# Optimization experiments

Measured on AMD Instinct MI355X. Metric: run time of the kernel, lower is better.

## Reference

```python
import jax, jax.numpy as jnp
import numpy as np

B, CIN, COUT, H, W, K, KH, KW = 32, 256, 256, 56, 56, 4, 3, 3
STRIDE, PAD = (1, 1), [(1, 1), (1, 1)]


def setup_inputs() -> dict:
    key = jax.random.key(0)
    ks = jax.random.split(key, 8)
    s_w = 1.0 / np.sqrt(CIN * KH * KW)
    return {
        "x": jax.random.normal(ks[0], (B, CIN, H, W), jnp.float32),
        "weight": jax.random.normal(ks[1], (K, COUT, CIN, KH, KW), jnp.float32) * s_w,
        "bias": jax.random.normal(ks[2], (K, COUT), jnp.float32) * s_w,
        "fc1_w": jax.random.normal(ks[3], (K, CIN), jnp.float32) / np.sqrt(CIN),
        "fc1_b": jax.random.normal(ks[4], (K,), jnp.float32) * 0.01,
        "fc2_w": jax.random.normal(ks[5], (K, K), jnp.float32) / np.sqrt(K),
        "fc2_b": jax.random.normal(ks[6], (K,), jnp.float32) * 0.01,
    }


def reference(x, weight, bias, fc1_w, fc1_b, fc2_w, fc2_b):
    # Attention2D: global avg pool -> 1x1 conv (dense) -> relu -> 1x1 conv -> softmax
    pooled = x.mean(axis=(2, 3))                                  # [B, CIN]
    a = jax.nn.relu(jnp.einsum('bc,kc->bk', pooled, fc1_w) + fc1_b)
    att = jax.nn.softmax(jnp.einsum('bk,jk->bj', a, fc2_w) + fc2_b, axis=1)  # [B, K]

    # Aggregate per-sample weights/bias over K experts
    agg_w = jnp.einsum('bk,koihw->boihw', att, weight)            # [B, COUT, CIN, KH, KW]
    agg_b = att @ bias                                            # [B, COUT]

    # Per-sample conv == grouped conv with groups=B in the torch original
    def conv_one(xi, wi):
        return jax.lax.conv_general_dilated(
            xi[None], wi, window_strides=STRIDE, padding=PAD,
            dimension_numbers=('NCHW', 'OIHW', 'NCHW'))[0]

    out = jax.vmap(conv_one)(x, agg_w)                            # [B, COUT, H, W]
    return out + agg_b[:, :, None, None]
```

## Files before the change

### kernel.cpp

```cpp
#include <hip/hip_runtime.h>
#include <hip/hip_bf16.h>
#include <stdint.h>

#define BB   32
#define CIN  256
#define COUT 256
#define HH   56
#define WW   56
#define HW   3136
#define KEXP 4
#define HP   58

typedef __attribute__((ext_vector_type(8))) short  short8;
typedef __attribute__((ext_vector_type(4))) float  floatx4;

__device__ __forceinline__ unsigned short f2bf(float f) {
    uint32_t u = __float_as_uint(f);
    u = (u + 0x7fffu + ((u >> 16) & 1u)) >> 16;
    return (unsigned short)u;
}
__device__ __forceinline__ float bf2f(unsigned short s) {
    return __uint_as_float(((uint32_t)s) << 16);
}
__device__ __forceinline__ uint32_t pack2(float a, float b) {
    return (uint32_t)f2bf(a) | ((uint32_t)f2bf(b) << 16);
}

__device__ __forceinline__ void async_copy16(const void* gsrc, void* ldst) {
    __builtin_amdgcn_global_load_lds(
        (const __attribute__((address_space(1))) unsigned int*)gsrc,
        (__attribute__((address_space(3))) unsigned int*)ldst, 16, 0, 0);
}

__global__ __launch_bounds__(256) void transpose_pool_kernel(
    const float* __restrict__ x,
    unsigned short* __restrict__ xt,
    float* __restrict__ partial)
{
    __shared__ unsigned short tile[CIN * 62];
    const int bx  = blockIdx.x;
    const int b   = bx / HH;
    const int h   = bx % HH;
    const int tid = threadIdx.x;

    const float* xb = x + (size_t)b * CIN * HW + h * WW;

    for (int i = tid; i < CIN * 14; i += 256) {
        const int c  = i / 14;
        const int wv = i % 14;
        const float4 v = *(const float4*)(xb + (size_t)c * HW + wv * 4);
        uint32_t* p = (uint32_t*)&tile[c * 62 + wv * 4];
        p[0] = pack2(v.x, v.y);
        p[1] = pack2(v.z, v.w);
    }
    __syncthreads();

    {
        float s = 0.f;
        #pragma unroll 8
        for (int i = 0; i < WW; ++i) s += bf2f(tile[tid * 62 + i]);
        partial[((size_t)b * HH + h) * CIN + tid] = s;
    }

    unsigned short* row = xt + (((size_t)b * HP + (h + 1)) * HP) * CIN;
    for (int j = tid; j < WW * 128; j += 256) {
        const int w  = j >> 7;
        const int c2 = (j & 127) * 2;
        const uint32_t v = (uint32_t)tile[c2 * 62 + w]
                         | ((uint32_t)tile[(c2 + 1) * 62 + w] << 16);
        *(uint32_t*)&row[(w + 1) * CIN + c2] = v;
    }

    if (tid < 128) {
        ((uint32_t*)&row[0])[tid]          = 0u;
        ((uint32_t*)&row[57 * CIN])[tid]   = 0u;
    }
    if (h == 0) {
        uint32_t* r0  = (uint32_t*)(xt + ((size_t)b * HP + 0)  * HP * CIN);
        uint32_t* r57 = (uint32_t*)(xt + ((size_t)b * HP + 57) * HP * CIN);
        for (int i = tid; i < HP * 128; i += 256) { r0[i] = 0u; r57[i] = 0u; }
    }
}

__global__ __launch_bounds__(256) void attn_kernel(
    const float* __restrict__ partial,
    const float* __restrict__ fc1w,
    const float* __restrict__ fc1b,
    const float* __restrict__ fc2w,
    const float* __restrict__ fc2b,
    float* __restrict__ att)
{
    __shared__ float pl[CIN];
    const int b   = blockIdx.x;
    const int tid = threadIdx.x;

    float s = 0.f;
    const float* pp = partial + (size_t)b * HH * CIN + tid;
    #pragma unroll 8
    for (int h = 0; h < HH; ++h) s += pp[h * CIN];
    pl[tid] = s * (1.0f / (float)HW);
    __syncthreads();

    if (tid < 64) {
        const int lane = tid;
        float sk[KEXP] = {0.f, 0.f, 0.f, 0.f};
        #pragma unroll
        for (int c0 = 0; c0 < CIN; c0 += 64) {
            const float p = pl[c0 + lane];
            #pragma unroll
            for (int k = 0; k < KEXP; ++k) sk[k] += p * fc1w[k * CIN + c0 + lane];
        }
        #pragma unroll
        for (int off = 32; off > 0; off >>= 1) {
            #pragma unroll
            for (int k = 0; k < KEXP; ++k) sk[k] += __shfl_down(sk[k], off);
        }
        if (lane == 0) {
            float a[KEXP];
            #pragma unroll
            for (int k = 0; k < KEXP; ++k) a[k] = fmaxf(sk[k] + fc1b[k], 0.f);
            float z[KEXP], m = -1e30f;
            #pragma unroll
            for (int j = 0; j < KEXP; ++j) {
                float t = fc2b[j];
                #pragma unroll
                for (int k = 0; k < KEXP; ++k) t += a[k] * fc2w[j * KEXP + k];
                z[j] = t;
                m = fmaxf(m, t);
            }
            float den = 0.f;
            #pragma unroll
            for (int j = 0; j < KEXP; ++j) { z[j] = expf(z[j] - m); den += z[j]; }
            const float inv = 1.0f / den;
            #pragma unroll
            for (int j = 0; j < KEXP; ++j) att[b * KEXP + j] = z[j] * inv;
        }
    }
}

__global__ __launch_bounds__(256) void aggw_kernel(
    const float* __restrict__ weight,
    const float* __restrict__ bias,
    const float* __restrict__ att,
    unsigned short* __restrict__ aggw,
    float* __restrict__ aggb)
{
    __shared__ float accw[CIN * 9];
    const int bx  = blockIdx.x;
    const int o   = bx >> 2;
    const int b0  = (bx & 3) * 8;
    const int tid = threadIdx.x;

    float wreg[KEXP][9];
    #pragma unroll
    for (int k = 0; k < KEXP; ++k) {
        const float* wk = weight + (size_t)(k * COUT + o) * (CIN * 9);
        #pragma unroll
        for (int j = 0; j < 9; ++j) wreg[k][j] = wk[j * 256 + tid];
    }
    float bvals[KEXP];
    #pragma unroll
    for (int k = 0; k < KEXP; ++k) bvals[k] = bias[k * COUT + o];

    for (int bi = 0; bi < 8; ++bi) {
        const int b = b0 + bi;
        float av[KEXP];
        #pragma unroll
        for (int k = 0; k < KEXP; ++k) av[k] = att[b * KEXP + k];

        __syncthreads();
        #pragma unroll
        for (int j = 0; j < 9; ++j) {
            float r = 0.f;
            #pragma unroll
            for (int k = 0; k < KEXP; ++k) r += av[k] * wreg[k][j];
            accw[j * 256 + tid] = r;
        }
        __syncthreads();

        for (int i = tid; i < 9 * 128; i += 256) {
            const int j  = i >> 7;
            const int cp = (i & 127) * 2;
            const uint32_t v = pack2(accw[cp * 9 + j], accw[(cp + 1) * 9 + j]);
            *(uint32_t*)&aggw[(((size_t)b * 9 + j) * COUT + o) * CIN + cp] = v;
        }
        if (tid == 0) {
            float sb = 0.f;
            #pragma unroll
            for (int k = 0; k < KEXP; ++k) sb += av[k] * bvals[k];
            aggb[b * COUT + o] = sb;
        }
    }
}

__global__ __launch_bounds__(256) void conv_gemm_kernel(
    const unsigned short* __restrict__ xt,
    const unsigned short* __restrict__ aggw,
    const float* __restrict__ aggb,
    float* __restrict__ out)
{
    __shared__ unsigned short As[128 * 64];
    __shared__ unsigned short Bs[128 * 64];

    const int bx   = blockIdx.x;
    const int slot = bx >> 3;
    const int xcd  = bx & 7;
    const int b    = xcd + 8 * (slot / 50);
    const int rr   = slot % 50;
    const int pt   = rr >> 1;
    const int ot   = rr & 1;
    const int o0   = ot * 128;
    const int p0   = pt * 128;

    const int tid  = threadIdx.x;
    const int wave = tid >> 6;
    const int lane = tid & 63;
    const int lrow = lane >> 3;
    const int lxor = ((lane & 7) ^ lrow) * 16;

    const char* aggw_b = (const char*)aggw + (size_t)b * 9 * COUT * CIN * 2;
    const char* xt_b   = (const char*)xt   + (size_t)b * HP * HP * CIN * 2;

    int aoff[4], boff[4];
    #pragma unroll
    for (int j = 0; j < 4; ++j) {
        const int rowl = j * 32 + wave * 8 + lrow;
        aoff[j] = (o0 + rowl) * 512 + lxor;
        const int p  = p0 + rowl;
        const int pv = (p < HW) ? p : 0;
        const int h  = pv / 56;
        const int w  = pv % 56;
        boff[j] = ((h + 1) * HP + (w + 1)) * 512 + lxor;
    }

    floatx4 acc[4][4];
    #pragma unroll
    for (int mi = 0; mi < 4; ++mi)
        #pragma unroll
        for (int ni = 0; ni < 4; ++ni)
            #pragma unroll
            for (int i = 0; i < 4; ++i) acc[mi][ni][i] = 0.f;

    const int row_base = (wave >> 1) * 64;
    const int col_base = (wave & 1) * 64;
    const int m_off    = lane & 15;
    const int q        = lane >> 4;
    const int sx       = m_off & 7;

    for (int kt = 0; kt < 36; ++kt) {
        const int rs = kt >> 2;
        const int c0 = (kt & 3) * 64;
        const int dh = rs / 3 - 1;
        const int dw = rs % 3 - 1;

        const int a_kt = rs * (COUT * CIN * 2) + c0 * 2;
        const int b_kt = (dh * HP + dw) * 512 + c0 * 2;

        #pragma unroll
        for (int j = 0; j < 4; ++j)
            async_copy16(aggw_b + (size_t)(aoff[j] + a_kt),
                         &As[(j * 32 + wave * 8) * 64]);
        #pragma unroll
        for (int j = 0; j < 4; ++j)
            async_copy16(xt_b + (size_t)(boff[j] + b_kt),
                         &Bs[(j * 32 + wave * 8) * 64]);
        __syncthreads();

        #pragma unroll
        for (int ks = 0; ks < 2; ++ks) {
            short8 af[4], bf[4];
            #pragma unroll
            for (int mi = 0; mi < 4; ++mi)
                af[mi] = *(const short8*)((const char*)As
                          + (row_base + mi * 16 + m_off) * 128
                          + (((ks * 4 + q) ^ sx) * 16));
            #pragma unroll
            for (int ni = 0; ni < 4; ++ni)
                bf[ni] = *(const short8*)((const char*)Bs
                          + (col_base + ni * 16 + m_off) * 128
                          + (((ks * 4 + q) ^ sx) * 16));
            #pragma unroll
            for (int mi = 0; mi < 4; ++mi)
                #pragma unroll
                for (int ni = 0; ni < 4; ++ni)
                    acc[mi][ni] = __builtin_amdgcn_mfma_f32_16x16x32_bf16(
                        af[mi], bf[ni], acc[mi][ni], 0, 0, 0);
        }
        __syncthreads();
    }

    float* outb = out + (size_t)b * COUT * HW;
    const int g4 = (lane >> 4) * 4;
    #pragma unroll
    for (int mi = 0; mi < 4; ++mi) {
        #pragma unroll
        for (int i = 0; i < 4; ++i) {
            const int o = o0 + row_base + mi * 16 + g4 + i;
            const float bv = aggb[b * COUT + o];
            #pragma unroll
            for (int ni = 0; ni < 4; ++ni) {
                const int p = p0 + col_base + ni * 16 + m_off;
                if (p < HW) outb[(size_t)o * HW + p] = acc[mi][ni][i] + bv;
            }
        }
    }
}

extern "C" void kernel_launch(void* const* d_in, const int* in_sizes, int n_in,
                              void* d_out, int out_size, void* d_ws, size_t ws_size,
                              hipStream_t stream) {
    const float* x      = (const float*)d_in[0];
    const float* weight = (const float*)d_in[1];
    const float* bias   = (const float*)d_in[2];
    const float* fc1w   = (const float*)d_in[3];
    const float* fc1b   = (const float*)d_in[4];
    const float* fc2w   = (const float*)d_in[5];
    const float* fc2b   = (const float*)d_in[6];
    float* out = (float*)d_out;

    char* ws = (char*)d_ws;
    unsigned short* xt      = (unsigned short*)(ws);
    unsigned short* aggw    = (unsigned short*)(ws + 55115776);
    float*          partial = (float*)(ws + 92864512);
    float*          att     = (float*)(ws + 94699520);
    float*          aggb    = (float*)(ws + 94700032);

    transpose_pool_kernel<<<BB * HH, 256, 0, stream>>>(x, xt, partial);
    attn_kernel<<<BB, 256, 0, stream>>>(partial, fc1w, fc1b, fc2w, fc2b, att);
    aggw_kernel<<<COUT * 4, 256, 0, stream>>>(weight, bias, att, aggw, aggb);
    conv_gemm_kernel<<<BB * 2 * 25, 256, 0, stream>>>(xt, aggw, aggb, out);
}
```

Baseline: 375.1 us.

## Rewrite conv GEMM with 256x256 tiles, double-buffered LDS and phased pipeline

The implicit-GEMM conv kernel moves from 128x128 tiles with 256 threads to 256x256 tiles with 512 threads (8 waves), so each workgroup covers all output channels. LDS is double-buffered at 128KB, and each k-step is split into four phases that interleave async global-to-LDS copies for upcoming steps with MFMA work, using s_barrier, vmcnt waits and setprio. The goal is to hide load latency and raise data reuse per tile. In exchange it uses more registers and LDS, so occupancy drops, and the 416-block grid may balance unevenly across CUs.

```diff
diff --git a/kernel.cpp b/kernel.cpp
--- a/kernel.cpp
+++ b/kernel.cpp
@@ -193,114 +193,143 @@
     }
 }
 
-__global__ __launch_bounds__(256) void conv_gemm_kernel(
+#define PHASE(MH, KS, LOADB, STAGE_STMT, VM_STMT) do {                         \
+    const char* Ap_ = lds + bufoff + (KS) * 16384 + lnoff;                     \
+    const char* Bp_ = lds + bufoff + 32768 + (KS) * 16384 + lnoff;             \
+    short8 af_[4];                                                             \
+    if (LOADB) {                                                               \
+        _Pragma("unroll")                                                      \
+        for (int ni_ = 0; ni_ < 4; ++ni_)                                      \
+            bf[ni_] = *(const short8*)(Bp_ + wn * 4096 + ni_ * 1024);          \
+    }                                                                          \
+    _Pragma("unroll")                                                          \
+    for (int mi_ = 0; mi_ < 4; ++mi_)                                          \
+        af_[mi_] = *(const short8*)(Ap_ + wm * 8192 + (MH) * 4096 + mi_ * 1024); \
+    STAGE_STMT;                                                                \
+    asm volatile("" ::: "memory");                                             \
+    __builtin_amdgcn_s_barrier();                                              \
+    asm volatile("" ::: "memory");                                             \
+    __builtin_amdgcn_s_setprio(1);                                             \
+    _Pragma("unroll")                                                          \
+    for (int mi_ = 0; mi_ < 4; ++mi_)                                          \
+        _Pragma("unroll")                                                      \
+        for (int ni_ = 0; ni_ < 4; ++ni_)                                      \
+            acc[(MH) * 4 + mi_][ni_] = __builtin_amdgcn_mfma_f32_16x16x32_bf16( \
+                af_[mi_], bf[ni_], acc[(MH) * 4 + mi_][ni_], 0, 0, 0);         \
+    __builtin_amdgcn_s_setprio(0);                                             \
+    VM_STMT;                                                                   \
+    asm volatile("" ::: "memory");                                             \
+    __builtin_amdgcn_s_barrier();                                              \
+    asm volatile("" ::: "memory");                                             \
+} while (0)
+
+__global__ __launch_bounds__(512, 2) void conv_gemm_kernel(
     const unsigned short* __restrict__ xt,
     const unsigned short* __restrict__ aggw,
     const float* __restrict__ aggb,
     float* __restrict__ out)
 {
-    __shared__ unsigned short As[128 * 64];
-    __shared__ unsigned short Bs[128 * 64];
-
-    const int bx   = blockIdx.x;
-    const int slot = bx >> 3;
-    const int xcd  = bx & 7;
-    const int b    = xcd + 8 * (slot / 50);
-    const int rr   = slot % 50;
-    const int pt   = rr >> 1;
-    const int ot   = rr & 1;
-    const int o0   = ot * 128;
-    const int p0   = pt * 128;
+    __shared__ __attribute__((aligned(128))) char lds[131072];
+
+    const int bx = blockIdx.x;
+    const int wg = (bx & 7) * 52 + (bx >> 3);
+    const int b  = wg / 13;
+    const int p0 = (wg - b * 13) * 256;
 
     const int tid  = threadIdx.x;
     const int wave = tid >> 6;
     const int lane = tid & 63;
-    const int lrow = lane >> 3;
-    const int lxor = ((lane & 7) ^ lrow) * 16;
-
-    const char* aggw_b = (const char*)aggw + (size_t)b * 9 * COUT * CIN * 2;
-    const char* xt_b   = (const char*)xt   + (size_t)b * HP * HP * CIN * 2;
-
-    int aoff[4], boff[4];
+    const int wm   = wave >> 2;
+    const int wn   = wave & 3;
+    const int m    = lane & 15;
+    const int q    = lane >> 4;
+    const int lnoff = m * 64 + ((q ^ (m >> 1)) & 3) * 16;
+
+    const char* aggw_b = (const char*)aggw + (size_t)b * (9 * COUT * CIN * 2);
+    const char* xt_b   = (const char*)xt   + (size_t)b * (HP * HP * CIN * 2);
+
+    int aoff0, aoff1, boff0, boff1;
+    {
+        int n = tid, r = n >> 2, u = n & 3, sw = (u ^ (r >> 1)) & 3;
+        aoff0 = r * 512 + sw * 16;
+        int p = p0 + r; int pv = (p < HW) ? p : 0;
+        int h = pv / WW, w = pv - h * WW;
+        boff0 = ((h + 1) * HP + (w + 1)) * 512 + sw * 16;
+
+        n = 512 + tid; r = n >> 2; u = n & 3; sw = (u ^ (r >> 1)) & 3;
+        aoff1 = r * 512 + sw * 16;
+        p = p0 + r; pv = (p < HW) ? p : 0;
+        h = pv / WW; w = pv - h * WW;
+        boff1 = ((h + 1) * HP + (w + 1)) * 512 + sw * 16;
+    }
+
+    auto stageA = [&](int kt, int ks) {
+        const int ga = (kt >> 2) * (COUT * CIN * 2) + (kt & 3) * 128 + ks * 64;
+        char* d = lds + (kt & 1) * 65536 + ks * 16384 + wave * 1024;
+        async_copy16(aggw_b + (ga + aoff0), d);
+        async_copy16(aggw_b + (ga + aoff1), d + 8192);
+    };
+    auto stageB = [&](int kt, int ks) {
+        const int rs = kt >> 2;
+        const int gb = ((rs / 3 - 1) * HP + (rs % 3 - 1)) * 512
+                     + (kt & 3) * 128 + ks * 64;
+        char* d = lds + (kt & 1) * 65536 + 32768 + ks * 16384 + wave * 1024;
+        async_copy16(xt_b + (gb + boff0), d);
+        async_copy16(xt_b + (gb + boff1), d + 8192);
+    };
+
+    floatx4 acc[8][4];
     #pragma unroll
-    for (int j = 0; j < 4; ++j) {
-        const int rowl = j * 32 + wave * 8 + lrow;
-        aoff[j] = (o0 + rowl) * 512 + lxor;
-        const int p  = p0 + rowl;
-        const int pv = (p < HW) ? p : 0;
-        const int h  = pv / 56;
-        const int w  = pv % 56;
-        boff[j] = ((h + 1) * HP + (w + 1)) * 512 + lxor;
-    }
-
-    floatx4 acc[4][4];
+    for (int a_ = 0; a_ < 8; ++a_)
+        #pragma unroll
+        for (int n_ = 0; n_ < 4; ++n_)
+            #pragma unroll
+            for (int e_ = 0; e_ < 4; ++e_) acc[a_][n_][e_] = 0.f;
+
+    stageA(0, 0); stageB(0, 0);
+    stageA(0, 1); stageB(0, 1);
+    stageA(1, 0); stageB(1, 0);
+    asm volatile("s_waitcnt vmcnt(4)" ::: "memory");
+    __builtin_amdgcn_s_barrier();
+    asm volatile("" ::: "memory");
+
+    #pragma unroll 1
+    for (int i = 0; i < 18; ++i) {
+        const int t0 = 2 * i;
+        {
+            const int bufoff = 0;
+            short8 bf[4];
+            PHASE(0, 0, 1, stageA(t0 + 1, 1), ((void)0));
+            PHASE(1, 0, 0, stageB(t0 + 1, 1), ((void)0));
+            PHASE(1, 1, 1, if (i < 17) stageA(t0 + 2, 0), ((void)0));
+            PHASE(0, 1, 0, if (i < 17) stageB(t0 + 2, 0),
+                  if (i < 17) { asm volatile("s_waitcnt vmcnt(4)" ::: "memory"); }
+                  else        { asm volatile("s_waitcnt vmcnt(0)" ::: "memory"); });
+        }
+        {
+            const int bufoff = 65536;
+            const int t1 = 2 * i + 1;
+            short8 bf[4];
+            PHASE(0, 0, 1, if (i < 17) stageA(t1 + 1, 1), ((void)0));
+            PHASE(1, 0, 0, if (i < 17) stageB(t1 + 1, 1), ((void)0));
+            PHASE(1, 1, 1, if (i < 17) stageA(t1 + 2, 0), ((void)0));
+            PHASE(0, 1, 0, if (i < 17) stageB(t1 + 2, 0),
+                  asm volatile("s_waitcnt vmcnt(4)" ::: "memory"));
+        }
+    }
+
+    float* outb = out + (size_t)b * COUT * HW;
+    const int g4 = q * 4;
     #pragma unroll
-    for (int mi = 0; mi < 4; ++mi)
-        #pragma unroll
-        for (int ni = 0; ni < 4; ++ni)
-            #pragma unroll
-            for (int i = 0; i < 4; ++i) acc[mi][ni][i] = 0.f;
-
-    const int row_base = (wave >> 1) * 64;
-    const int col_base = (wave & 1) * 64;
-    const int m_off    = lane & 15;
-    const int q        = lane >> 4;
-    const int sx       = m_off & 7;
-
-    for (int kt = 0; kt < 36; ++kt) {
-        const int rs = kt >> 2;
-        const int c0 = (kt & 3) * 64;
-        const int dh = rs / 3 - 1;
-        const int dw = rs % 3 - 1;
-
-        const int a_kt = rs * (COUT * CIN * 2) + c0 * 2;
-        const int b_kt = (dh * HP + dw) * 512 + c0 * 2;
-
-        #pragma unroll
-        for (int j = 0; j < 4; ++j)
-            async_copy16(aggw_b + (size_t)(aoff[j] + a_kt),
-                         &As[(j * 32 + wave * 8) * 64]);
-        #pragma unroll
-        for (int j = 0; j < 4; ++j)
-            async_copy16(xt_b + (size_t)(boff[j] + b_kt),
-                         &Bs[(j * 32 + wave * 8) * 64]);
-        __syncthreads();
-
-        #pragma unroll
-        for (int ks = 0; ks < 2; ++ks) {
-            short8 af[4], bf[4];
-            #pragma unroll
-            for (int mi = 0; mi < 4; ++mi)
-                af[mi] = *(const short8*)((const char*)As
-                          + (row_base + mi * 16 + m_off) * 128
-                          + (((ks * 4 + q) ^ sx) * 16));
-            #pragma unroll
-            for (int ni = 0; ni < 4; ++ni)
-                bf[ni] = *(const short8*)((const char*)Bs
-                          + (col_base + ni * 16 + m_off) * 128
-                          + (((ks * 4 + q) ^ sx) * 16));
-            #pragma unroll
-            for (int mi = 0; mi < 4; ++mi)
-                #pragma unroll
-                for (int ni = 0; ni < 4; ++ni)
-                    acc[mi][ni] = __builtin_amdgcn_mfma_f32_16x16x32_bf16(
-                        af[mi], bf[ni], acc[mi][ni], 0, 0, 0);
-        }
-        __syncthreads();
-    }
-
-    float* outb = out + (size_t)b * COUT * HW;
-    const int g4 = (lane >> 4) * 4;
-    #pragma unroll
-    for (int mi = 0; mi < 4; ++mi) {
-        #pragma unroll
-        for (int i = 0; i < 4; ++i) {
-            const int o = o0 + row_base + mi * 16 + g4 + i;
-            const float bv = aggb[b * COUT + o];
+    for (int am = 0; am < 8; ++am) {
+        const int o = wm * 128 + am * 16 + g4;
+        #pragma unroll
+        for (int e = 0; e < 4; ++e) {
+            const float bv = aggb[b * COUT + o + e];
             #pragma unroll
             for (int ni = 0; ni < 4; ++ni) {
-                const int p = p0 + col_base + ni * 16 + m_off;
-                if (p < HW) outb[(size_t)o * HW + p] = acc[mi][ni][i] + bv;
+                const int p = p0 + wn * 64 + ni * 16 + m;
+                if (p < HW) outb[(size_t)(o + e) * HW + p] = acc[am][ni][e] + bv;
             }
         }
     }
@@ -328,5 +357,5 @@
     transpose_pool_kernel<<<BB * HH, 256, 0, stream>>>(x, xt, partial);
     attn_kernel<<<BB, 256, 0, stream>>>(partial, fc1w, fc1b, fc2w, fc2b, att);
     aggw_kernel<<<COUT * 4, 256, 0, stream>>>(weight, bias, att, aggw, aggb);
-    conv_gemm_kernel<<<BB * 2 * 25, 256, 0, stream>>>(xt, aggw, aggb, out);
-}
+    conv_gemm_kernel<<<BB * 13, 512, 0, stream>>>(xt, aggw, aggb, out);
+}
```

After: 366.0 us. 2.4% less time.
